# Optimization experiments

Hardware: AMD Instinct MI355X
Metric: run time of the kernel (lower is better)

## Reference

```python
import jax, jax.numpy as jnp
import numpy as np

N, E, B, D, H, C = 50000, 800000, 128, 64, 128, 2
EPS = 1e-5


def setup_inputs() -> dict:
    key = jax.random.key(0)
    ks = jax.random.split(key, 12)
    s = 0.1
    return {
        "x": jax.random.normal(ks[0], (N, D), jnp.float32),
        "edge_index": jax.random.randint(ks[1], (2, E), 0, N, jnp.int64),
        "batch": jnp.sort(jax.random.randint(ks[2], (N,), 0, B, jnp.int64)),
        "W_l": jax.random.normal(ks[3], (D, D), jnp.float32) * s,
        "b_l": jnp.zeros((D,), jnp.float32),
        "W_r": jax.random.normal(ks[4], (D, D), jnp.float32) * s,
        "W_res": jax.random.normal(ks[5], (D, D), jnp.float32) * s,
        "b_res": jnp.zeros((D,), jnp.float32),
        "gamma": jnp.ones((D,), jnp.float32),
        "beta": jnp.zeros((D,), jnp.float32),
        "gate_W1": jax.random.normal(ks[6], (D, D), jnp.float32) * s,
        "gate_b1": jnp.zeros((D,), jnp.float32),
        "gate_W2": jax.random.normal(ks[7], (D, 1), jnp.float32) * s,
        "gate_b2": jnp.zeros((1,), jnp.float32),
        "W_p1": jax.random.normal(ks[8], (D, H), jnp.float32) * s,
        "b_p1": jnp.zeros((H,), jnp.float32),
        "W_p2": jax.random.normal(ks[9], (H, C), jnp.float32) * s,
        "b_p2": jnp.zeros((C,), jnp.float32),
    }


def reference(x, edge_index, batch, W_l, b_l, W_r, W_res, b_res, gamma, beta,
              gate_W1, gate_b1, gate_W2, gate_b2, W_p1, b_p1, W_p2, b_p2):
    src, dst = edge_index[0], edge_index[1]
    # SAGEConv, mean aggregation: gather source feats, scatter-mean to target
    agg = jax.ops.segment_sum(x[src], dst, num_segments=N)          # [N, D]
    cnt = jax.ops.segment_sum(jnp.ones((E,), x.dtype), dst, num_segments=N)
    mean = agg / jnp.maximum(cnt, 1.0)[:, None]
    h = mean @ W_l + b_l + x @ W_r                                   # [N, D]
    # dropout is identity (eval mode)
    # BatchNorm1d (training-mode math: biased batch stats)
    mu = jnp.mean(h, axis=0)
    var = jnp.var(h, axis=0)
    h = (h - mu) * jax.lax.rsqrt(var + EPS) * gamma + beta
    # residual projection of the original features
    h = h + x @ W_res + b_res
    # GlobalAttention pooling: per-graph softmax over gate scores
    gate = jax.nn.relu(h @ gate_W1 + gate_b1) @ gate_W2 + gate_b2    # [N, 1]
    g = gate[:, 0]
    gmax = jax.ops.segment_max(g, batch, num_segments=B)
    gmax = jnp.where(jnp.isfinite(gmax), gmax, 0.0)
    e = jnp.exp(g - gmax[batch])
    z = jax.ops.segment_sum(e, batch, num_segments=B)
    alpha = e / jnp.maximum(z, 1e-16)[batch]
    pooled = jax.ops.segment_sum(alpha[:, None] * h, batch, num_segments=B)  # [B, D]
    # 2-layer predictor MLP with ReLU between
    out = jax.nn.relu(pooled @ W_p1 + b_p1) @ W_p2 + b_p2            # [B, C]
    return out
```

## Files before the change

kernel.cpp:

```cpp
#include <hip/hip_runtime.h>
#include <math.h>

#define N_NODES 50000
#define N_EDGES 800000
#define BATCHES 128
#define DIM 64
#define HID 128
#define NCLS 2
#define EPSV 1e-5f
#define MAXD 64

#define NPART 8
#define PART_SZ ((N_NODES + NPART - 1) / NPART)
#define EPB 2048
#define NCHK_E ((N_EDGES + EPB - 1) / EPB)
#define NCHUNK1 782

typedef __attribute__((ext_vector_type(8))) short bf16x8;
typedef __attribute__((ext_vector_type(4))) float f32x4;

__device__ __forceinline__ unsigned short f2bf(float f){
  unsigned u = __float_as_uint(f);
  u += 0x7FFFu + ((u >> 16) & 1u);
  return (unsigned short)(u >> 16);
}
__device__ __forceinline__ float bf2f(unsigned short h){
  return __uint_as_float(((unsigned)h) << 16);
}
__device__ __forceinline__ void split2(float f, unsigned short& hi, unsigned short& lo){
  hi = f2bf(f);
  lo = f2bf(f - bf2f(hi));
}
__device__ __forceinline__ uint4 pack8(const unsigned short* s){
  uint4 u;
  u.x = (unsigned)s[0] | ((unsigned)s[1] << 16);
  u.y = (unsigned)s[2] | ((unsigned)s[3] << 16);
  u.z = (unsigned)s[4] | ((unsigned)s[5] << 16);
  u.w = (unsigned)s[6] | ((unsigned)s[7] << 16);
  return u;
}

__global__ void k_scatter(const int* __restrict__ ei, int* __restrict__ cnt,
                          unsigned short* __restrict__ csr){
  const int p = blockIdx.x & (NPART-1);
  const int c = blockIdx.x >> 3;
  const int lo = p * PART_SZ;
  const int hi = lo + PART_SZ;
  const int e0 = c * EPB;
  const int e1 = (e0 + EPB < N_EDGES) ? e0 + EPB : N_EDGES;
  for (int i = e0 + threadIdx.x; i < e1; i += 256){
    int d = ei[N_EDGES + i];
    if (d >= lo && d < hi){
      int s = ei[i];
      int pos = atomicAdd(&cnt[d], 1);
      csr[(size_t)d*MAXD + pos] = (unsigned short)s;
    }
  }
}

__global__ void k_mean(const float* __restrict__ x,
                       const unsigned short* __restrict__ csr,
                       const int* __restrict__ cnt, float* __restrict__ meanb){
  const int node = (blockIdx.x*256 + threadIdx.x) >> 6;
  const int lane = threadIdx.x & 63;
  const int g = lane >> 4, f = lane & 15;
  const int dg = cnt[node];
  const size_t start = (size_t)node * MAXD;
  float4 acc = make_float4(0.f,0.f,0.f,0.f);
  int e = (lane < dg) ? (int)csr[start + lane] : 0;
  int i = 0;
  for (; i + 16 <= dg; i += 16){
    int s0 = __shfl(e, i +      g, 64);
    int s1 = __shfl(e, i + 4  + g, 64);
    int s2 = __shfl(e, i + 8  + g, 64);
    int s3 = __shfl(e, i + 12 + g, 64);
    float4 v0 = *(const float4*)&x[(size_t)s0*DIM + f*4];
    float4 v1 = *(const float4*)&x[(size_t)s1*DIM + f*4];
    float4 v2 = *(const float4*)&x[(size_t)s2*DIM + f*4];
    float4 v3 = *(const float4*)&x[(size_t)s3*DIM + f*4];
    acc.x += v0.x + v1.x + v2.x + v3.x;
    acc.y += v0.y + v1.y + v2.y + v3.y;
    acc.z += v0.z + v1.z + v2.z + v3.z;
    acc.w += v0.w + v1.w + v2.w + v3.w;
  }
  for (; i < dg; i += 4){
    int idx = i + g;
    int srcl = (idx < dg) ? idx : (dg - 1);
    int s = __shfl(e, srcl, 64);
    if (idx < dg){
      float4 v = *(const float4*)&x[(size_t)s*DIM + f*4];
      acc.x += v.x; acc.y += v.y; acc.z += v.z; acc.w += v.w;
    }
  }
  acc.x += __shfl_xor(acc.x, 16, 64); acc.x += __shfl_xor(acc.x, 32, 64);
  acc.y += __shfl_xor(acc.y, 16, 64); acc.y += __shfl_xor(acc.y, 32, 64);
  acc.z += __shfl_xor(acc.z, 16, 64); acc.z += __shfl_xor(acc.z, 32, 64);
  acc.w += __shfl_xor(acc.w, 16, 64); acc.w += __shfl_xor(acc.w, 32, 64);
  if (g == 0){
    float inv = 1.f / fmaxf((float)dg, 1.f);
    float4 r = make_float4(acc.x*inv, acc.y*inv, acc.z*inv, acc.w*inv);
    *(float4*)&meanb[(size_t)node*DIM + f*4] = r;
  }
}

__global__ void __launch_bounds__(256) k_lin1(
    const float* __restrict__ meanb, const float* __restrict__ x,
    const float* __restrict__ Wl, const float* __restrict__ bl,
    const float* __restrict__ Wr, float* __restrict__ hbuf,
    float* __restrict__ pstat){
  __shared__ __align__(16) short sB[2][64][136];
  __shared__ __align__(16) short sA[2][64][72];
  const int tid  = threadIdx.x;
  const int lane = tid & 63, w = tid >> 6;
  const int jc   = lane & 15;
  const int mrow = 16*w + jc;
  const int koff = (lane >> 4) * 8;
  const int r0   = 16*w + (lane >> 4)*4;
  const int base = blockIdx.x * 64;

  {
    const int k0 = 32 * w;
    #pragma unroll
    for (int kc = 0; kc < 4; ++kc){
      unsigned short h[8], l[8];
      #pragma unroll
      for (int i = 0; i < 8; ++i){
        int k = k0 + 8*kc + i;
        float v = (k < 64) ? Wl[k*DIM + lane] : Wr[(k-64)*DIM + lane];
        split2(v, h[i], l[i]);
      }
      *(uint4*)&sB[0][lane][k0 + 8*kc] = pack8(h);
      *(uint4*)&sB[1][lane][k0 + 8*kc] = pack8(l);
    }
  }

  float blv[4];
  #pragma unroll
  for (int nt = 0; nt < 4; ++nt) blv[nt] = bl[nt*16 + jc];

  f32x4 acc[4] = {};
  #pragma unroll
  for (int half = 0; half < 2; ++half){
    const float* __restrict__ src = half ? x : meanb;
    __syncthreads();
    {
      const int row = tid >> 2;
      const int kq  = (tid & 3) * 16;
      const int node = base + row;
      #pragma unroll
      for (int cc = 0; cc < 4; ++cc){
        float4 v = make_float4(0.f,0.f,0.f,0.f);
        if (node < N_NODES) v = *(const float4*)&src[(size_t)node*DIM + kq + 4*cc];
        unsigned short h[4], l[4];
        split2(v.x,h[0],l[0]); split2(v.y,h[1],l[1]);
        split2(v.z,h[2],l[2]); split2(v.w,h[3],l[3]);
        uint2 ph, pl;
        ph.x = (unsigned)h[0] | ((unsigned)h[1]<<16);
        ph.y = (unsigned)h[2] | ((unsigned)h[3]<<16);
        pl.x = (unsigned)l[0] | ((unsigned)l[1]<<16);
        pl.y = (unsigned)l[2] | ((unsigned)l[3]<<16);
        *(uint2*)&sA[0][row][kq + 4*cc] = ph;
        *(uint2*)&sA[1][row][kq + 4*cc] = pl;
      }
    }
    __syncthreads();
    #pragma unroll
    for (int kt2 = 0; kt2 < 2; ++kt2){
      const int ka = kt2*32 + koff;
      const int kb = half*64 + ka;
      bf16x8 ah = *(const bf16x8*)&sA[0][mrow][ka];
      bf16x8 al = *(const bf16x8*)&sA[1][mrow][ka];
      #pragma unroll
      for (int nt = 0; nt < 4; ++nt){
        const int nr = nt*16 + jc;
        bf16x8 bh = *(const bf16x8*)&sB[0][nr][kb];
        bf16x8 bo = *(const bf16x8*)&sB[1][nr][kb];
        acc[nt] = __builtin_amdgcn_mfma_f32_16x16x32_bf16(ah, bh, acc[nt], 0,0,0);
        acc[nt] = __builtin_amdgcn_mfma_f32_16x16x32_bf16(al, bh, acc[nt], 0,0,0);
        acc[nt] = __builtin_amdgcn_mfma_f32_16x16x32_bf16(ah, bo, acc[nt], 0,0,0);
      }
    }
  }

  float s1[4] = {0.f,0.f,0.f,0.f}, s2[4] = {0.f,0.f,0.f,0.f};
  #pragma unroll
  for (int nt = 0; nt < 4; ++nt){
    const int col = nt*16 + jc;
    #pragma unroll
    for (int r = 0; r < 4; ++r){
      const int node = base + r0 + r;
      float v = acc[nt][r] + blv[nt];
      if (node < N_NODES){
        hbuf[(size_t)node*DIM + col] = v;
        s1[nt] += v; s2[nt] += v*v;
      }
    }
  }

  __syncthreads();
  float* sred = (float*)sA;
  #pragma unroll
  for (int nt = 0; nt < 4; ++nt){
    float a = s1[nt], b = s2[nt];
    a += __shfl_xor(a, 16, 64); a += __shfl_xor(a, 32, 64);
    b += __shfl_xor(b, 16, 64); b += __shfl_xor(b, 32, 64);
    if ((lane >> 4) == 0){
      sred[0*256 + w*64 + nt*16 + jc] = a;
      sred[1*256 + w*64 + nt*16 + jc] = b;
    }
  }
  __syncthreads();
  if (tid < 64){
    float a = sred[tid] + sred[64+tid] + sred[128+tid] + sred[192+tid];
    float b = sred[256+tid] + sred[320+tid] + sred[384+tid] + sred[448+tid];
    pstat[(size_t)blockIdx.x*128 + tid]      = a;
    pstat[(size_t)blockIdx.x*128 + 64 + tid] = b;
  }
}

__global__ void __launch_bounds__(256) k_stats(
    const float* __restrict__ pstat, float* __restrict__ muinv){
  __shared__ float r1[256], r2[256];
  const int j = blockIdx.x;
  const int t = threadIdx.x;
  float s1 = 0.f, s2 = 0.f;
  for (int c = t; c < NCHUNK1; c += 256){
    s1 += pstat[(size_t)c*128 + j];
    s2 += pstat[(size_t)c*128 + 64 + j];
  }
  r1[t] = s1; r2[t] = s2;
  __syncthreads();
  for (int st = 128; st > 0; st >>= 1){
    if (t < st){ r1[t] += r1[t+st]; r2[t] += r2[t+st]; }
    __syncthreads();
  }
  if (t == 0){
    float mu = r1[0] / (float)N_NODES;
    float var = r2[0] / (float)N_NODES - mu*mu;
    muinv[j] = mu;
    muinv[DIM+j] = 1.0f / sqrtf(var + EPSV);
  }
}

__device__ __forceinline__ void stage_w64(short* sWh, short* sWl_,
                                          const float* __restrict__ W,
                                          int w, int lane){
  const int k0 = 16 * w;
  #pragma unroll
  for (int kc = 0; kc < 2; ++kc){
    unsigned short h[8], l[8];
    #pragma unroll
    for (int i = 0; i < 8; ++i){
      int k = k0 + 8*kc + i;
      split2(W[k*DIM + lane], h[i], l[i]);
    }
    *(uint4*)&sWh[lane*72 + k0 + 8*kc] = pack8(h);
    *(uint4*)&sWl_[lane*72 + k0 + 8*kc] = pack8(l);
  }
}

__global__ void __launch_bounds__(256) k_lin2(
    const float* __restrict__ x, const float* __restrict__ hbuf,
    const float* __restrict__ Wres, const float* __restrict__ bres,
    const float* __restrict__ gamma, const float* __restrict__ beta,
    const float* __restrict__ muinv,
    const float* __restrict__ gW1, const float* __restrict__ gb1,
    const float* __restrict__ gW2, const float* __restrict__ gb2,
    const int* __restrict__ batch,
    float* __restrict__ zbuf, float* __restrict__ pooled){
  __shared__ __align__(16) short sW[2][64][72];
  __shared__ __align__(16) short sA[2][64][72];
  __shared__ int sb[64];
  __shared__ unsigned long long runmask;
  const int tid  = threadIdx.x;
  const int lane = tid & 63, w = tid >> 6;
  const int jc   = lane & 15;
  const int g16  = w*4 + (lane >> 4);
  const int mrow = 16*w + jc;
  const int koff = (lane >> 4) * 8;
  const int r0   = 16*w + (lane >> 4)*4;
  const int base = blockIdx.x * 64;

  float muv[4], invv[4], gav[4], bev[4], brv[4], g1v[4], w2v[4];
  #pragma unroll
  for (int nt = 0; nt < 4; ++nt){
    const int col = nt*16 + jc;
    muv[nt] = muinv[col];  invv[nt] = muinv[DIM+col];
    gav[nt] = gamma[col];  bev[nt]  = beta[col];
    brv[nt] = bres[col];   g1v[nt]  = gb1[col];
    w2v[nt] = gW2[col];
  }
  const float gb2v = gb2[0];

  {
    const int row = tid >> 2;
    const int kq  = (tid & 3) * 16;
    const int node = base + row;
    #pragma unroll
    for (int cc = 0; cc < 4; ++cc){
      float4 v = make_float4(0.f,0.f,0.f,0.f);
      if (node < N_NODES) v = *(const float4*)&x[(size_t)node*DIM + kq + 4*cc];
      unsigned short h[4], l[4];
      split2(v.x,h[0],l[0]); split2(v.y,h[1],l[1]);
      split2(v.z,h[2],l[2]); split2(v.w,h[3],l[3]);
      uint2 ph, pl;
      ph.x = (unsigned)h[0] | ((unsigned)h[1]<<16);
      ph.y = (unsigned)h[2] | ((unsigned)h[3]<<16);
      pl.x = (unsigned)l[0] | ((unsigned)l[1]<<16);
      pl.y = (unsigned)l[2] | ((unsigned)l[3]<<16);
      *(uint2*)&sA[0][row][kq + 4*cc] = ph;
      *(uint2*)&sA[1][row][kq + 4*cc] = pl;
    }
  }
  if (tid < 64){
    int nn = base + tid;
    sb[tid] = batch[(nn < N_NODES) ? nn : (N_NODES-1)];
  }
  stage_w64(&sW[0][0][0], &sW[1][0][0], Wres, w, lane);
  __syncthreads();

  if (w == 0){
    bool fl = (lane > 0) && (sb[lane] != sb[lane-1]);
    unsigned long long mm = __ballot(fl);
    if (lane == 0) runmask = mm;
  }

  f32x4 acc[4] = {};
  #pragma unroll
  for (int kt2 = 0; kt2 < 2; ++kt2){
    const int ka = kt2*32 + koff;
    bf16x8 ah = *(const bf16x8*)&sA[0][mrow][ka];
    bf16x8 al = *(const bf16x8*)&sA[1][mrow][ka];
    #pragma unroll
    for (int nt = 0; nt < 4; ++nt){
      const int nr = nt*16 + jc;
      bf16x8 bh = *(const bf16x8*)&sW[0][nr][ka];
      bf16x8 bo = *(const bf16x8*)&sW[1][nr][ka];
      acc[nt] = __builtin_amdgcn_mfma_f32_16x16x32_bf16(ah, bh, acc[nt], 0,0,0);
      acc[nt] = __builtin_amdgcn_mfma_f32_16x16x32_bf16(al, bh, acc[nt], 0,0,0);
      acc[nt] = __builtin_amdgcn_mfma_f32_16x16x32_bf16(ah, bo, acc[nt], 0,0,0);
    }
  }

  float vk[4][4];
  #pragma unroll
  for (int nt = 0; nt < 4; ++nt){
    const int col = nt*16 + jc;
    #pragma unroll
    for (int r = 0; r < 4; ++r){
      const int node = base + r0 + r;
      float hp = 0.f;
      if (node < N_NODES) hp = hbuf[(size_t)node*DIM + col];
      float v = (hp - muv[nt])*invv[nt]*gav[nt] + bev[nt] + brv[nt] + acc[nt][r];
      vk[nt][r] = v;
      unsigned short hh, ll;
      split2(v, hh, ll);
      sA[0][r0 + r][col] = (short)hh;
      sA[1][r0 + r][col] = (short)ll;
    }
  }
  __syncthreads();
  stage_w64(&sW[0][0][0], &sW[1][0][0], gW1, w, lane);
  __syncthreads();

  f32x4 acc2[4] = {};
  #pragma unroll
  for (int kt2 = 0; kt2 < 2; ++kt2){
    const int ka = kt2*32 + koff;
    bf16x8 ah = *(const bf16x8*)&sA[0][mrow][ka];
    bf16x8 al = *(const bf16x8*)&sA[1][mrow][ka];
    #pragma unroll
    for (int nt = 0; nt < 4; ++nt){
      const int nr = nt*16 + jc;
      bf16x8 bh = *(const bf16x8*)&sW[0][nr][ka];
      bf16x8 bo = *(const bf16x8*)&sW[1][nr][ka];
      acc2[nt] = __builtin_amdgcn_mfma_f32_16x16x32_bf16(ah, bh, acc2[nt], 0,0,0);
      acc2[nt] = __builtin_amdgcn_mfma_f32_16x16x32_bf16(al, bh, acc2[nt], 0,0,0);
      acc2[nt] = __builtin_amdgcn_mfma_f32_16x16x32_bf16(ah, bo, acc2[nt], 0,0,0);
    }
  }

  float p[4] = {0.f,0.f,0.f,0.f};
  #pragma unroll
  for (int nt = 0; nt < 4; ++nt){
    #pragma unroll
    for (int r = 0; r < 4; ++r)
      p[r] += fmaxf(acc2[nt][r] + g1v[nt], 0.f) * w2v[nt];
  }
  float ev[4];
  #pragma unroll
  for (int r = 0; r < 4; ++r){
    float t = p[r];
    t += __shfl_xor(t, 1, 64); t += __shfl_xor(t, 2, 64);
    t += __shfl_xor(t, 4, 64); t += __shfl_xor(t, 8, 64);
    const int node = base + r0 + r;
    ev[r] = (node < N_NODES) ? expf(t + gb2v) : 0.f;
  }

  float* sredp = (float*)&sA[0][0][0];
  float* szl   = sredp + 16*64;
  __syncthreads();
  const unsigned long long m = runmask;
  int rstart = 0;
  while (rstart < 64){
    const int bseg = sb[rstart];
    unsigned long long rest = (rstart >= 63) ? 0ull : (m >> (rstart+1));
    const int rend = rest ? (rstart + 1 + __builtin_ctzll(rest)) : 64;
    float pacc[4] = {0.f,0.f,0.f,0.f};
    float zacc = 0.f;
    #pragma unroll
    for (int r = 0; r < 4; ++r){
      const int ln = 4*g16 + r;
      if (ln >= rstart && ln < rend){
        #pragma unroll
        for (int nt = 0; nt < 4; ++nt) pacc[nt] += ev[r]*vk[nt][r];
        zacc += ev[r];
      }
    }
    #pragma unroll
    for (int nt = 0; nt < 4; ++nt) sredp[g16*64 + nt*16 + jc] = pacc[nt];
    if ((lane & 15) == 0) szl[g16] = zacc;
    __syncthreads();
    if (tid < 64){
      float s = 0.f;
      #pragma unroll 4
      for (int g2 = 0; g2 < 16; ++g2) s += sredp[g2*64 + tid];
      atomicAdd(&pooled[bseg*DIM + tid], s);
    }
    if (tid == 64){
      float sz2 = 0.f;
      for (int g2 = 0; g2 < 16; ++g2) sz2 += szl[g2];
      atomicAdd(&zbuf[bseg], sz2);
    }
    __syncthreads();
    rstart = rend;
  }
}

__global__ void k_head(const float* __restrict__ pooled, const float* __restrict__ zbuf,
                       const float* __restrict__ Wp1, const float* __restrict__ bp1,
                       const float* __restrict__ Wp2, const float* __restrict__ bp2,
                       float* __restrict__ out){
  __shared__ float ps[DIM];
  __shared__ float red[4];
  int b = blockIdx.x;
  int t = threadIdx.x;
  if (t < DIM){
    float zz = fmaxf(zbuf[b], 1e-16f);
    ps[t] = pooled[b*DIM + t] / zz;
  }
  __syncthreads();
  float acc = bp1[t];
  #pragma unroll
  for (int d2=0; d2<DIM; d2++) acc = fmaf(ps[d2], Wp1[d2*HID + t], acc);
  acc = fmaxf(acc, 0.f);
  float o0 = acc * Wp2[t*NCLS+0];
  float o1 = acc * Wp2[t*NCLS+1];
  #pragma unroll
  for (int o=32;o>0;o>>=1){ o0 += __shfl_down(o0,o,64); o1 += __shfl_down(o1,o,64); }
  int w = t>>6;
  if ((t&63)==0){ red[w*2+0]=o0; red[w*2+1]=o1; }
  __syncthreads();
  if (t==0){
    out[b*NCLS+0] = red[0]+red[2]+bp2[0];
    out[b*NCLS+1] = red[1]+red[3]+bp2[1];
  }
}

extern "C" void kernel_launch(void* const* d_in, const int* in_sizes, int n_in,
                              void* d_out, int out_size, void* d_ws, size_t ws_size,
                              hipStream_t stream){
  const float* x     = (const float*)d_in[0];
  const int*   ei    = (const int*)d_in[1];
  const int*   batch = (const int*)d_in[2];
  const float* Wl    = (const float*)d_in[3];
  const float* bl    = (const float*)d_in[4];
  const float* Wr    = (const float*)d_in[5];
  const float* Wres  = (const float*)d_in[6];
  const float* bres  = (const float*)d_in[7];
  const float* gamma = (const float*)d_in[8];
  const float* beta  = (const float*)d_in[9];
  const float* gW1   = (const float*)d_in[10];
  const float* gb1   = (const float*)d_in[11];
  const float* gW2   = (const float*)d_in[12];
  const float* gb2   = (const float*)d_in[13];
  const float* Wp1   = (const float*)d_in[14];
  const float* bp1   = (const float*)d_in[15];
  const float* Wp2   = (const float*)d_in[16];
  const float* bp2   = (const float*)d_in[17];
  float* outp = (float*)d_out;

  int*   cnt   = (int*)d_ws;
  float* zbuf  = (float*)(cnt + N_NODES);
  float* pooled= zbuf + BATCHES;
  float* pstat = pooled + (size_t)BATCHES*DIM;
  float* muinv = pstat + (size_t)NCHUNK1*128;
  float* meanb = muinv + 2*DIM;
  float* hbuf  = meanb + (size_t)N_NODES*DIM;
  unsigned short* csr = (unsigned short*)(hbuf + (size_t)N_NODES*DIM);

  const size_t zcount = (size_t)N_NODES + BATCHES + (size_t)BATCHES*DIM;
  hipMemsetAsync(d_ws, 0, zcount*sizeof(int), stream);

  k_scatter<<<NPART*NCHK_E, 256, 0, stream>>>(ei, cnt, csr);
  k_mean   <<<N_NODES/4, 256, 0, stream>>>(x, csr, cnt, meanb);
  k_lin1   <<<NCHUNK1, 256, 0, stream>>>(meanb, x, Wl, bl, Wr, hbuf, pstat);
  k_stats  <<<64, 256, 0, stream>>>(pstat, muinv);
  k_lin2   <<<NCHUNK1, 256, 0, stream>>>(x, hbuf, Wres, bres, gamma, beta, muinv,
                                         gW1, gb1, gW2, gb2, batch, zbuf, pooled);
  k_head   <<<BATCHES, HID, 0, stream>>>(pooled, zbuf, Wp1, bp1, Wp2, bp2, outp);
}
```

Baseline: 200.7 us.

## Fuse lin1, stats, lin2 and head into one persistent kernel with grid barriers

Merges the four post-aggregation kernels into a single kernel of 782 blocks that synchronises through software grid barriers built on atomic counters. The pre-norm activations stay in registers instead of going out to a global h buffer and being read back. BatchNorm statistics are accumulated with atomics into replicated, strided slots instead of per-block partials plus a separate reduction kernel. This removes three launches and the hbuf round trip, but it depends on all 782 blocks being co-resident (launch bounds 256,4); if they are not, the spin barriers can deadlock.

```diff
diff --git a/kernel.cpp b/kernel.cpp
--- a/kernel.cpp
+++ b/kernel.cpp
@@ -14,7 +14,10 @@
 #define PART_SZ ((N_NODES + NPART - 1) / NPART)
 #define EPB 2048
 #define NCHK_E ((N_EDGES + EPB - 1) / EPB)
-#define NCHUNK1 782
+#define NBLK 782
+
+#define MREP 4
+#define MSTRIDE 32
 
 typedef __attribute__((ext_vector_type(8))) short bf16x8;
 typedef __attribute__((ext_vector_type(4))) float f32x4;
@@ -38,6 +41,22 @@
   u.z = (unsigned)s[4] | ((unsigned)s[5] << 16);
   u.w = (unsigned)s[6] | ((unsigned)s[7] << 16);
   return u;
+}
+
+__device__ __forceinline__ float gload(const float* p){
+  return __hip_atomic_load(p, __ATOMIC_RELAXED, __HIP_MEMORY_SCOPE_AGENT);
+}
+
+__device__ __forceinline__ void gbar(unsigned* c){
+  __syncthreads();
+  if (threadIdx.x == 0){
+    __hip_atomic_fetch_add(c, 1u, __ATOMIC_ACQ_REL, __HIP_MEMORY_SCOPE_AGENT);
+    while (__hip_atomic_load(c, __ATOMIC_RELAXED, __HIP_MEMORY_SCOPE_AGENT)
+           < (unsigned)NBLK)
+      __builtin_amdgcn_s_sleep(8);
+    __builtin_amdgcn_fence(__ATOMIC_ACQUIRE, "agent");
+  }
+  __syncthreads();
 }
 
 __global__ void k_scatter(const int* __restrict__ ei, int* __restrict__ cnt,
@@ -103,145 +122,6 @@
   }
 }
 
-__global__ void __launch_bounds__(256) k_lin1(
-    const float* __restrict__ meanb, const float* __restrict__ x,
-    const float* __restrict__ Wl, const float* __restrict__ bl,
-    const float* __restrict__ Wr, float* __restrict__ hbuf,
-    float* __restrict__ pstat){
-  __shared__ __align__(16) short sB[2][64][136];
-  __shared__ __align__(16) short sA[2][64][72];
-  const int tid  = threadIdx.x;
-  const int lane = tid & 63, w = tid >> 6;
-  const int jc   = lane & 15;
-  const int mrow = 16*w + jc;
-  const int koff = (lane >> 4) * 8;
-  const int r0   = 16*w + (lane >> 4)*4;
-  const int base = blockIdx.x * 64;
-
-  {
-    const int k0 = 32 * w;
-    #pragma unroll
-    for (int kc = 0; kc < 4; ++kc){
-      unsigned short h[8], l[8];
-      #pragma unroll
-      for (int i = 0; i < 8; ++i){
-        int k = k0 + 8*kc + i;
-        float v = (k < 64) ? Wl[k*DIM + lane] : Wr[(k-64)*DIM + lane];
-        split2(v, h[i], l[i]);
-      }
-      *(uint4*)&sB[0][lane][k0 + 8*kc] = pack8(h);
-      *(uint4*)&sB[1][lane][k0 + 8*kc] = pack8(l);
-    }
-  }
-
-  float blv[4];
-  #pragma unroll
-  for (int nt = 0; nt < 4; ++nt) blv[nt] = bl[nt*16 + jc];
-
-  f32x4 acc[4] = {};
-  #pragma unroll
-  for (int half = 0; half < 2; ++half){
-    const float* __restrict__ src = half ? x : meanb;
-    __syncthreads();
-    {
-      const int row = tid >> 2;
-      const int kq  = (tid & 3) * 16;
-      const int node = base + row;
-      #pragma unroll
-      for (int cc = 0; cc < 4; ++cc){
-        float4 v = make_float4(0.f,0.f,0.f,0.f);
-        if (node < N_NODES) v = *(const float4*)&src[(size_t)node*DIM + kq + 4*cc];
-        unsigned short h[4], l[4];
-        split2(v.x,h[0],l[0]); split2(v.y,h[1],l[1]);
-        split2(v.z,h[2],l[2]); split2(v.w,h[3],l[3]);
-        uint2 ph, pl;
-        ph.x = (unsigned)h[0] | ((unsigned)h[1]<<16);
-        ph.y = (unsigned)h[2] | ((unsigned)h[3]<<16);
-        pl.x = (unsigned)l[0] | ((unsigned)l[1]<<16);
-        pl.y = (unsigned)l[2] | ((unsigned)l[3]<<16);
-        *(uint2*)&sA[0][row][kq + 4*cc] = ph;
-        *(uint2*)&sA[1][row][kq + 4*cc] = pl;
-      }
-    }
-    __syncthreads();
-    #pragma unroll
-    for (int kt2 = 0; kt2 < 2; ++kt2){
-      const int ka = kt2*32 + koff;
-      const int kb = half*64 + ka;
-      bf16x8 ah = *(const bf16x8*)&sA[0][mrow][ka];
-      bf16x8 al = *(const bf16x8*)&sA[1][mrow][ka];
-      #pragma unroll
-      for (int nt = 0; nt < 4; ++nt){
-        const int nr = nt*16 + jc;
-        bf16x8 bh = *(const bf16x8*)&sB[0][nr][kb];
-        bf16x8 bo = *(const bf16x8*)&sB[1][nr][kb];
-        acc[nt] = __builtin_amdgcn_mfma_f32_16x16x32_bf16(ah, bh, acc[nt], 0,0,0);
-        acc[nt] = __builtin_amdgcn_mfma_f32_16x16x32_bf16(al, bh, acc[nt], 0,0,0);
-        acc[nt] = __builtin_amdgcn_mfma_f32_16x16x32_bf16(ah, bo, acc[nt], 0,0,0);
-      }
-    }
-  }
-
-  float s1[4] = {0.f,0.f,0.f,0.f}, s2[4] = {0.f,0.f,0.f,0.f};
-  #pragma unroll
-  for (int nt = 0; nt < 4; ++nt){
-    const int col = nt*16 + jc;
-    #pragma unroll
-    for (int r = 0; r < 4; ++r){
-      const int node = base + r0 + r;
-      float v = acc[nt][r] + blv[nt];
-      if (node < N_NODES){
-        hbuf[(size_t)node*DIM + col] = v;
-        s1[nt] += v; s2[nt] += v*v;
-      }
-    }
-  }
-
-  __syncthreads();
-  float* sred = (float*)sA;
-  #pragma unroll
-  for (int nt = 0; nt < 4; ++nt){
-    float a = s1[nt], b = s2[nt];
-    a += __shfl_xor(a, 16, 64); a += __shfl_xor(a, 32, 64);
-    b += __shfl_xor(b, 16, 64); b += __shfl_xor(b, 32, 64);
-    if ((lane >> 4) == 0){
-      sred[0*256 + w*64 + nt*16 + jc] = a;
-      sred[1*256 + w*64 + nt*16 + jc] = b;
-    }
-  }
-  __syncthreads();
-  if (tid < 64){
-    float a = sred[tid] + sred[64+tid] + sred[128+tid] + sred[192+tid];
-    float b = sred[256+tid] + sred[320+tid] + sred[384+tid] + sred[448+tid];
-    pstat[(size_t)blockIdx.x*128 + tid]      = a;
-    pstat[(size_t)blockIdx.x*128 + 64 + tid] = b;
-  }
-}
-
-__global__ void __launch_bounds__(256) k_stats(
-    const float* __restrict__ pstat, float* __restrict__ muinv){
-  __shared__ float r1[256], r2[256];
-  const int j = blockIdx.x;
-  const int t = threadIdx.x;
-  float s1 = 0.f, s2 = 0.f;
-  for (int c = t; c < NCHUNK1; c += 256){
-    s1 += pstat[(size_t)c*128 + j];
-    s2 += pstat[(size_t)c*128 + 64 + j];
-  }
-  r1[t] = s1; r2[t] = s2;
-  __syncthreads();
-  for (int st = 128; st > 0; st >>= 1){
-    if (t < st){ r1[t] += r1[t+st]; r2[t] += r2[t+st]; }
-    __syncthreads();
-  }
-  if (t == 0){
-    float mu = r1[0] / (float)N_NODES;
-    float var = r2[0] / (float)N_NODES - mu*mu;
-    muinv[j] = mu;
-    muinv[DIM+j] = 1.0f / sqrtf(var + EPSV);
-  }
-}
-
 __device__ __forceinline__ void stage_w64(short* sWh, short* sWl_,
                                           const float* __restrict__ W,
                                           int w, int lane){
@@ -259,19 +139,67 @@
   }
 }
 
-__global__ void __launch_bounds__(256) k_lin2(
-    const float* __restrict__ x, const float* __restrict__ hbuf,
+#define GEMM64(ACC) do { \
+  _Pragma("unroll") \
+  for (int kt2 = 0; kt2 < 2; ++kt2){ \
+    const int ka = kt2*32 + koff; \
+    bf16x8 ah = *(const bf16x8*)&sA[0][mrow][ka]; \
+    bf16x8 al = *(const bf16x8*)&sA[1][mrow][ka]; \
+    _Pragma("unroll") \
+    for (int nt = 0; nt < 4; ++nt){ \
+      const int nr = nt*16 + jc; \
+      bf16x8 bh = *(const bf16x8*)&sB[0][nr][ka]; \
+      bf16x8 bo = *(const bf16x8*)&sB[1][nr][ka]; \
+      ACC[nt] = __builtin_amdgcn_mfma_f32_16x16x32_bf16(ah, bh, ACC[nt], 0,0,0); \
+      ACC[nt] = __builtin_amdgcn_mfma_f32_16x16x32_bf16(al, bh, ACC[nt], 0,0,0); \
+      ACC[nt] = __builtin_amdgcn_mfma_f32_16x16x32_bf16(ah, bo, ACC[nt], 0,0,0); \
+    } \
+  } \
+} while(0)
+
+#define STAGE_A(SRC) do { \
+  const int row_  = tid >> 2; \
+  const int kq_   = (tid & 3) * 16; \
+  const int node_ = base + row_; \
+  _Pragma("unroll") \
+  for (int cc = 0; cc < 4; ++cc){ \
+    float4 v = make_float4(0.f,0.f,0.f,0.f); \
+    if (node_ < N_NODES) v = *(const float4*)&SRC[(size_t)node_*DIM + kq_ + 4*cc]; \
+    unsigned short h_[4], l_[4]; \
+    split2(v.x,h_[0],l_[0]); split2(v.y,h_[1],l_[1]); \
+    split2(v.z,h_[2],l_[2]); split2(v.w,h_[3],l_[3]); \
+    uint2 ph_, pl_; \
+    ph_.x = (unsigned)h_[0] | ((unsigned)h_[1]<<16); \
+    ph_.y = (unsigned)h_[2] | ((unsigned)h_[3]<<16); \
+    pl_.x = (unsigned)l_[0] | ((unsigned)l_[1]<<16); \
+    pl_.y = (unsigned)l_[2] | ((unsigned)l_[3]<<16); \
+    *(uint2*)&sA[0][row_][kq_ + 4*cc] = ph_; \
+    *(uint2*)&sA[1][row_][kq_ + 4*cc] = pl_; \
+  } \
+} while(0)
+
+__global__ void __launch_bounds__(256, 4) k_mega(
+    const float* __restrict__ meanb, const float* __restrict__ x,
+    const float* __restrict__ Wl, const float* __restrict__ bl,
+    const float* __restrict__ Wr,
     const float* __restrict__ Wres, const float* __restrict__ bres,
     const float* __restrict__ gamma, const float* __restrict__ beta,
-    const float* __restrict__ muinv,
     const float* __restrict__ gW1, const float* __restrict__ gb1,
     const float* __restrict__ gW2, const float* __restrict__ gb2,
+    const float* __restrict__ Wp1, const float* __restrict__ bp1,
+    const float* __restrict__ Wp2, const float* __restrict__ bp2,
     const int* __restrict__ batch,
-    float* __restrict__ zbuf, float* __restrict__ pooled){
-  __shared__ __align__(16) short sW[2][64][72];
+    float* __restrict__ musum,
+    float* __restrict__ zbuf, float* __restrict__ pooled,
+    unsigned* __restrict__ bar, float* __restrict__ outp){
   __shared__ __align__(16) short sA[2][64][72];
+  __shared__ __align__(16) short sB[2][64][72];
   __shared__ int sb[64];
   __shared__ unsigned long long runmask;
+  __shared__ float smu[2*DIM];
+  __shared__ float psh[DIM];
+  __shared__ float redh[4];
+
   const int tid  = threadIdx.x;
   const int lane = tid & 63, w = tid >> 6;
   const int jc   = lane & 15;
@@ -279,80 +207,105 @@
   const int mrow = 16*w + jc;
   const int koff = (lane >> 4) * 8;
   const int r0   = 16*w + (lane >> 4)*4;
-  const int base = blockIdx.x * 64;
+  const int bx   = blockIdx.x;
+  const int base = bx * 64;
+
+  float blv[4];
+  #pragma unroll
+  for (int nt = 0; nt < 4; ++nt) blv[nt] = bl[nt*16 + jc];
+
+  f32x4 acc[4] = {};
+  stage_w64(&sB[0][0][0], &sB[1][0][0], Wl, w, lane);
+  STAGE_A(meanb);
+  __syncthreads();
+  GEMM64(acc);
+  __syncthreads();
+  stage_w64(&sB[0][0][0], &sB[1][0][0], Wr, w, lane);
+  STAGE_A(x);
+  __syncthreads();
+  GEMM64(acc);
+
+  float s1v[4] = {0.f,0.f,0.f,0.f}, s2v[4] = {0.f,0.f,0.f,0.f};
+  #pragma unroll
+  for (int nt = 0; nt < 4; ++nt){
+    #pragma unroll
+    for (int r = 0; r < 4; ++r){
+      const int node = base + r0 + r;
+      float v = acc[nt][r] + blv[nt];
+      acc[nt][r] = v;
+      if (node < N_NODES){ s1v[nt] += v; s2v[nt] += v*v; }
+    }
+  }
+  __syncthreads();
+  {
+    float* sred = (float*)&sB[0][0][0];
+    #pragma unroll
+    for (int nt = 0; nt < 4; ++nt){
+      float a = s1v[nt], b = s2v[nt];
+      a += __shfl_xor(a, 16, 64); a += __shfl_xor(a, 32, 64);
+      b += __shfl_xor(b, 16, 64); b += __shfl_xor(b, 32, 64);
+      if ((lane >> 4) == 0){
+        sred[0*256 + w*64 + nt*16 + jc] = a;
+        sred[1*256 + w*64 + nt*16 + jc] = b;
+      }
+    }
+    __syncthreads();
+    const int rep = bx & (MREP-1);
+    if (tid < 64){
+      float a = sred[tid] + sred[64+tid] + sred[128+tid] + sred[192+tid];
+      float b = sred[256+tid] + sred[320+tid] + sred[384+tid] + sred[448+tid];
+      atomicAdd(&musum[(size_t)rep*128*MSTRIDE + (size_t)tid*MSTRIDE], a);
+      atomicAdd(&musum[(size_t)rep*128*MSTRIDE + (size_t)(64+tid)*MSTRIDE], b);
+    }
+  }
+  gbar(&bar[0]);
+
+  if (tid < 64){
+    float s1 = 0.f, s2 = 0.f;
+    #pragma unroll
+    for (int rep = 0; rep < MREP; ++rep){
+      s1 += gload(&musum[(size_t)rep*128*MSTRIDE + (size_t)tid*MSTRIDE]);
+      s2 += gload(&musum[(size_t)rep*128*MSTRIDE + (size_t)(64+tid)*MSTRIDE]);
+    }
+    float mu = s1 / (float)N_NODES;
+    float var = s2 / (float)N_NODES - mu*mu;
+    smu[tid] = mu;
+    smu[DIM+tid] = 1.0f / sqrtf(var + EPSV);
+  }
+  if (tid < 64){
+    int nn = base + tid;
+    sb[tid] = batch[(nn < N_NODES) ? nn : (N_NODES-1)];
+  }
+  stage_w64(&sB[0][0][0], &sB[1][0][0], Wres, w, lane);
+  __syncthreads();
 
   float muv[4], invv[4], gav[4], bev[4], brv[4], g1v[4], w2v[4];
   #pragma unroll
   for (int nt = 0; nt < 4; ++nt){
     const int col = nt*16 + jc;
-    muv[nt] = muinv[col];  invv[nt] = muinv[DIM+col];
+    muv[nt] = smu[col];    invv[nt] = smu[DIM+col];
     gav[nt] = gamma[col];  bev[nt]  = beta[col];
     brv[nt] = bres[col];   g1v[nt]  = gb1[col];
     w2v[nt] = gW2[col];
   }
   const float gb2v = gb2[0];
-
-  {
-    const int row = tid >> 2;
-    const int kq  = (tid & 3) * 16;
-    const int node = base + row;
-    #pragma unroll
-    for (int cc = 0; cc < 4; ++cc){
-      float4 v = make_float4(0.f,0.f,0.f,0.f);
-      if (node < N_NODES) v = *(const float4*)&x[(size_t)node*DIM + kq + 4*cc];
-      unsigned short h[4], l[4];
-      split2(v.x,h[0],l[0]); split2(v.y,h[1],l[1]);
-      split2(v.z,h[2],l[2]); split2(v.w,h[3],l[3]);
-      uint2 ph, pl;
-      ph.x = (unsigned)h[0] | ((unsigned)h[1]<<16);
-      ph.y = (unsigned)h[2] | ((unsigned)h[3]<<16);
-      pl.x = (unsigned)l[0] | ((unsigned)l[1]<<16);
-      pl.y = (unsigned)l[2] | ((unsigned)l[3]<<16);
-      *(uint2*)&sA[0][row][kq + 4*cc] = ph;
-      *(uint2*)&sA[1][row][kq + 4*cc] = pl;
-    }
-  }
-  if (tid < 64){
-    int nn = base + tid;
-    sb[tid] = batch[(nn < N_NODES) ? nn : (N_NODES-1)];
-  }
-  stage_w64(&sW[0][0][0], &sW[1][0][0], Wres, w, lane);
-  __syncthreads();
-
   if (w == 0){
     bool fl = (lane > 0) && (sb[lane] != sb[lane-1]);
     unsigned long long mm = __ballot(fl);
     if (lane == 0) runmask = mm;
   }
 
-  f32x4 acc[4] = {};
-  #pragma unroll
-  for (int kt2 = 0; kt2 < 2; ++kt2){
-    const int ka = kt2*32 + koff;
-    bf16x8 ah = *(const bf16x8*)&sA[0][mrow][ka];
-    bf16x8 al = *(const bf16x8*)&sA[1][mrow][ka];
-    #pragma unroll
-    for (int nt = 0; nt < 4; ++nt){
-      const int nr = nt*16 + jc;
-      bf16x8 bh = *(const bf16x8*)&sW[0][nr][ka];
-      bf16x8 bo = *(const bf16x8*)&sW[1][nr][ka];
-      acc[nt] = __builtin_amdgcn_mfma_f32_16x16x32_bf16(ah, bh, acc[nt], 0,0,0);
-      acc[nt] = __builtin_amdgcn_mfma_f32_16x16x32_bf16(al, bh, acc[nt], 0,0,0);
-      acc[nt] = __builtin_amdgcn_mfma_f32_16x16x32_bf16(ah, bo, acc[nt], 0,0,0);
-    }
-  }
-
-  float vk[4][4];
+  f32x4 acc2[4] = {};
+  GEMM64(acc2);
+
   #pragma unroll
   for (int nt = 0; nt < 4; ++nt){
     const int col = nt*16 + jc;
     #pragma unroll
     for (int r = 0; r < 4; ++r){
-      const int node = base + r0 + r;
-      float hp = 0.f;
-      if (node < N_NODES) hp = hbuf[(size_t)node*DIM + col];
-      float v = (hp - muv[nt])*invv[nt]*gav[nt] + bev[nt] + brv[nt] + acc[nt][r];
-      vk[nt][r] = v;
+      float v = (acc[nt][r] - muv[nt])*invv[nt]*gav[nt] + bev[nt]
+              + brv[nt] + acc2[nt][r];
+      acc[nt][r] = v;
       unsigned short hh, ll;
       split2(v, hh, ll);
       sA[0][r0 + r][col] = (short)hh;
@@ -360,32 +313,18 @@
     }
   }
   __syncthreads();
-  stage_w64(&sW[0][0][0], &sW[1][0][0], gW1, w, lane);
-  __syncthreads();
-
-  f32x4 acc2[4] = {};
-  #pragma unroll
-  for (int kt2 = 0; kt2 < 2; ++kt2){
-    const int ka = kt2*32 + koff;
-    bf16x8 ah = *(const bf16x8*)&sA[0][mrow][ka];
-    bf16x8 al = *(const bf16x8*)&sA[1][mrow][ka];
-    #pragma unroll
-    for (int nt = 0; nt < 4; ++nt){
-      const int nr = nt*16 + jc;
-      bf16x8 bh = *(const bf16x8*)&sW[0][nr][ka];
-      bf16x8 bo = *(const bf16x8*)&sW[1][nr][ka];
-      acc2[nt] = __builtin_amdgcn_mfma_f32_16x16x32_bf16(ah, bh, acc2[nt], 0,0,0);
-      acc2[nt] = __builtin_amdgcn_mfma_f32_16x16x32_bf16(al, bh, acc2[nt], 0,0,0);
-      acc2[nt] = __builtin_amdgcn_mfma_f32_16x16x32_bf16(ah, bo, acc2[nt], 0,0,0);
-    }
-  }
+  stage_w64(&sB[0][0][0], &sB[1][0][0], gW1, w, lane);
+  __syncthreads();
+
+  f32x4 acc3[4] = {};
+  GEMM64(acc3);
 
   float p[4] = {0.f,0.f,0.f,0.f};
   #pragma unroll
   for (int nt = 0; nt < 4; ++nt){
     #pragma unroll
     for (int r = 0; r < 4; ++r)
-      p[r] += fmaxf(acc2[nt][r] + g1v[nt], 0.f) * w2v[nt];
+      p[r] += fmaxf(acc3[nt][r] + g1v[nt], 0.f) * w2v[nt];
   }
   float ev[4];
   #pragma unroll
@@ -397,73 +336,74 @@
     ev[r] = (node < N_NODES) ? expf(t + gb2v) : 0.f;
   }
 
-  float* sredp = (float*)&sA[0][0][0];
-  float* szl   = sredp + 16*64;
-  __syncthreads();
-  const unsigned long long m = runmask;
-  int rstart = 0;
-  while (rstart < 64){
-    const int bseg = sb[rstart];
-    unsigned long long rest = (rstart >= 63) ? 0ull : (m >> (rstart+1));
-    const int rend = rest ? (rstart + 1 + __builtin_ctzll(rest)) : 64;
-    float pacc[4] = {0.f,0.f,0.f,0.f};
-    float zacc = 0.f;
-    #pragma unroll
-    for (int r = 0; r < 4; ++r){
-      const int ln = 4*g16 + r;
-      if (ln >= rstart && ln < rend){
-        #pragma unroll
-        for (int nt = 0; nt < 4; ++nt) pacc[nt] += ev[r]*vk[nt][r];
-        zacc += ev[r];
+  {
+    float* sredp = (float*)&sA[0][0][0];
+    float* szl   = sredp + 16*64;
+    __syncthreads();
+    const unsigned long long m = runmask;
+    int rstart = 0;
+    while (rstart < 64){
+      const int bseg = sb[rstart];
+      unsigned long long rest = (rstart >= 63) ? 0ull : (m >> (rstart+1));
+      const int rend = rest ? (rstart + 1 + __builtin_ctzll(rest)) : 64;
+      float pacc[4] = {0.f,0.f,0.f,0.f};
+      float zacc = 0.f;
+      #pragma unroll
+      for (int r = 0; r < 4; ++r){
+        const int ln = 4*g16 + r;
+        if (ln >= rstart && ln < rend){
+          #pragma unroll
+          for (int nt = 0; nt < 4; ++nt) pacc[nt] += ev[r]*acc[nt][r];
+          zacc += ev[r];
+        }
       }
-    }
-    #pragma unroll
-    for (int nt = 0; nt < 4; ++nt) sredp[g16*64 + nt*16 + jc] = pacc[nt];
-    if ((lane & 15) == 0) szl[g16] = zacc;
+      #pragma unroll
+      for (int nt = 0; nt < 4; ++nt) sredp[g16*64 + nt*16 + jc] = pacc[nt];
+      if ((lane & 15) == 0) szl[g16] = zacc;
+      __syncthreads();
+      if (tid < 64){
+        float s = 0.f;
+        for (int g2 = 0; g2 < 16; ++g2) s += sredp[g2*64 + tid];
+        atomicAdd(&pooled[bseg*DIM + tid], s);
+      }
+      if (tid == 64){
+        float sz2 = 0.f;
+        for (int g2 = 0; g2 < 16; ++g2) sz2 += szl[g2];
+        atomicAdd(&zbuf[bseg], sz2);
+      }
+      __syncthreads();
+      rstart = rend;
+    }
+  }
+  gbar(&bar[1]);
+
+  if (bx < BATCHES){
+    const int b = bx;
+    const int t = tid;
+    if (t < DIM){
+      float zz = fmaxf(gload(&zbuf[b]), 1e-16f);
+      psh[t] = gload(&pooled[b*DIM + t]) / zz;
+    }
     __syncthreads();
-    if (tid < 64){
-      float s = 0.f;
-      #pragma unroll 4
-      for (int g2 = 0; g2 < 16; ++g2) s += sredp[g2*64 + tid];
-      atomicAdd(&pooled[bseg*DIM + tid], s);
-    }
-    if (tid == 64){
-      float sz2 = 0.f;
-      for (int g2 = 0; g2 < 16; ++g2) sz2 += szl[g2];
-      atomicAdd(&zbuf[bseg], sz2);
+    if (t < HID){
+      float a = bp1[t];
+      #pragma unroll
+      for (int d2 = 0; d2 < DIM; ++d2) a = fmaf(psh[d2], Wp1[d2*HID + t], a);
+      a = fmaxf(a, 0.f);
+      float o0 = a * Wp2[t*NCLS+0];
+      float o1 = a * Wp2[t*NCLS+1];
+      #pragma unroll
+      for (int o = 32; o > 0; o >>= 1){
+        o0 += __shfl_down(o0, o, 64); o1 += __shfl_down(o1, o, 64);
+      }
+      int hw = t >> 6;
+      if ((t & 63) == 0){ redh[hw*2+0] = o0; redh[hw*2+1] = o1; }
     }
     __syncthreads();
-    rstart = rend;
-  }
-}
-
-__global__ void k_head(const float* __restrict__ pooled, const float* __restrict__ zbuf,
-                       const float* __restrict__ Wp1, const float* __restrict__ bp1,
-                       const float* __restrict__ Wp2, const float* __restrict__ bp2,
-                       float* __restrict__ out){
-  __shared__ float ps[DIM];
-  __shared__ float red[4];
-  int b = blockIdx.x;
-  int t = threadIdx.x;
-  if (t < DIM){
-    float zz = fmaxf(zbuf[b], 1e-16f);
-    ps[t] = pooled[b*DIM + t] / zz;
-  }
-  __syncthreads();
-  float acc = bp1[t];
-  #pragma unroll
-  for (int d2=0; d2<DIM; d2++) acc = fmaf(ps[d2], Wp1[d2*HID + t], acc);
-  acc = fmaxf(acc, 0.f);
-  float o0 = acc * Wp2[t*NCLS+0];
-  float o1 = acc * Wp2[t*NCLS+1];
-  #pragma unroll
-  for (int o=32;o>0;o>>=1){ o0 += __shfl_down(o0,o,64); o1 += __shfl_down(o1,o,64); }
-  int w = t>>6;
-  if ((t&63)==0){ red[w*2+0]=o0; red[w*2+1]=o1; }
-  __syncthreads();
-  if (t==0){
-    out[b*NCLS+0] = red[0]+red[2]+bp2[0];
-    out[b*NCLS+1] = red[1]+red[3]+bp2[1];
+    if (t == 0){
+      outp[b*NCLS+0] = redh[0]+redh[2]+bp2[0];
+      outp[b*NCLS+1] = redh[1]+redh[3]+bp2[1];
+    }
   }
 }
 
@@ -490,23 +430,22 @@
   const float* bp2   = (const float*)d_in[17];
   float* outp = (float*)d_out;
 
-  int*   cnt   = (int*)d_ws;
-  float* zbuf  = (float*)(cnt + N_NODES);
-  float* pooled= zbuf + BATCHES;
-  float* pstat = pooled + (size_t)BATCHES*DIM;
-  float* muinv = pstat + (size_t)NCHUNK1*128;
-  float* meanb = muinv + 2*DIM;
-  float* hbuf  = meanb + (size_t)N_NODES*DIM;
-  unsigned short* csr = (unsigned short*)(hbuf + (size_t)N_NODES*DIM);
-
-  const size_t zcount = (size_t)N_NODES + BATCHES + (size_t)BATCHES*DIM;
+  int*      cnt    = (int*)d_ws;
+  float*    zbuf   = (float*)(cnt + N_NODES);
+  float*    pooled = zbuf + BATCHES;
+  unsigned* bar    = (unsigned*)(pooled + (size_t)BATCHES*DIM);
+  float*    musum  = (float*)(bar + 8);
+  float*    meanb  = musum + (size_t)MREP*128*MSTRIDE;
+  unsigned short* csr = (unsigned short*)(meanb + (size_t)N_NODES*DIM);
+
+  const size_t zcount = (size_t)N_NODES + BATCHES + (size_t)BATCHES*DIM + 8
+                      + (size_t)MREP*128*MSTRIDE;
   hipMemsetAsync(d_ws, 0, zcount*sizeof(int), stream);
 
   k_scatter<<<NPART*NCHK_E, 256, 0, stream>>>(ei, cnt, csr);
   k_mean   <<<N_NODES/4, 256, 0, stream>>>(x, csr, cnt, meanb);
-  k_lin1   <<<NCHUNK1, 256, 0, stream>>>(meanb, x, Wl, bl, Wr, hbuf, pstat);
-  k_stats  <<<64, 256, 0, stream>>>(pstat, muinv);
-  k_lin2   <<<NCHUNK1, 256, 0, stream>>>(x, hbuf, Wres, bres, gamma, beta, muinv,
-                                         gW1, gb1, gW2, gb2, batch, zbuf, pooled);
-  k_head   <<<BATCHES, HID, 0, stream>>>(pooled, zbuf, Wp1, bp1, Wp2, bp2, outp);
-}
+  k_mega   <<<NBLK, 256, 0, stream>>>(meanb, x, Wl, bl, Wr, Wres, bres,
+                                      gamma, beta, gW1, gb1, gW2, gb2,
+                                      Wp1, bp1, Wp2, bp2, batch,
+                                      musum, zbuf, pooled, bar, outp);
+}
```

Result: slower. 270.9 us (+35.0%).
